# Optimization experiments

Measured on AMD Instinct MI355X. Metric: run time of the kernel, lower is better.

The kernel has to match this reference:

```python
import jax, jax.numpy as jnp
import numpy as np

B, N, C = 4, 2048, 1024
H = 16
HD = C // H
SCALE = HD ** -0.5


def setup_inputs() -> dict:
    key = jax.random.key(0)
    k1, k2, k3, k4 = jax.random.split(key, 4)
    x = jax.random.normal(k1, (B, N, C), dtype=jnp.float32)
    w_qkv = jax.random.normal(k2, (3 * C, C), dtype=jnp.float32) * (C ** -0.5)
    w_proj = jax.random.normal(k3, (C, C), dtype=jnp.float32) * (C ** -0.5)
    b_proj = jax.random.normal(k4, (C,), dtype=jnp.float32) * 0.01
    return {"x": x, "w_qkv": w_qkv, "w_proj": w_proj, "b_proj": b_proj}


def reference(x, w_qkv, w_proj, b_proj):
    qkv = jnp.einsum('bnc,dc->bnd', x, w_qkv)
    qkv = qkv.reshape(B, N, 3, H, HD).transpose(2, 0, 3, 1, 4)
    q, k, v = qkv[0], qkv[1], qkv[2]
    # scaled dot-product attention with explicit softmax (dropout p=0 -> identity)
    attn = jnp.einsum('bhqd,bhkd->bhqk', q, k) * SCALE
    attn = jax.nn.softmax(attn, axis=-1)
    out = jnp.einsum('bhqk,bhkd->bhqd', attn, v)
    out = out.transpose(0, 2, 1, 3).reshape(B, N, C)
    # output projection
    return jnp.einsum('bnc,dc->bnd', out, w_proj) + b_proj
```

## Files before the change

### kernel.cpp

```cpp
#include <hip/hip_runtime.h>

typedef unsigned short u16;
typedef unsigned int u32;
typedef __bf16 bf16x8 __attribute__((ext_vector_type(8)));
typedef __bf16 bf16x4 __attribute__((ext_vector_type(4)));
typedef short s16x4 __attribute__((ext_vector_type(4)));
typedef float f32x4 __attribute__((ext_vector_type(4)));
typedef float f32x16 __attribute__((ext_vector_type(16)));
typedef unsigned int u32x2 __attribute__((ext_vector_type(2)));
typedef unsigned int u32x4 __attribute__((ext_vector_type(4)));

struct __align__(8) u16x4 { u16 x, y, z, w; };

__device__ __forceinline__ void async_copy16(const void* g, void* l) {
  __builtin_amdgcn_global_load_lds(
      (__attribute__((address_space(1))) void*)g,
      (__attribute__((address_space(3))) void*)l, 16, 0, 0);
}

__device__ __forceinline__ u16 f2bf(float f) {
  unsigned u = __builtin_bit_cast(unsigned, f);
  u = (u + 0x7FFFu + ((u >> 16) & 1u)) >> 16;
  return (u16)u;
}
__device__ __forceinline__ float bf2f(u16 h) {
  unsigned u = ((unsigned)h) << 16;
  return __builtin_bit_cast(float, u);
}

__device__ __forceinline__ float fast_exp2(float x) {
  return __builtin_amdgcn_exp2f(x);
}
__device__ __forceinline__ float fast_rcp(float x) {
  return __builtin_amdgcn_rcpf(x);
}

__device__ __forceinline__ f32x4 mfma32(bf16x8 a, bf16x8 b, f32x4 c) {
  return __builtin_amdgcn_mfma_f32_16x16x32_bf16(a, b, c, 0, 0, 0);
}

__device__ __forceinline__ u32 cvt_pk_bf16(float lo, float hi) {
  u32 r;
  asm("v_cvt_pk_bf16_f32 %0, %1, %2" : "=v"(r) : "v"(lo), "v"(hi));
  return r;
}

#define CEXP 0.18033688011112042f

__global__ void detect_mode(const u32* __restrict__ probe, int* __restrict__ flag) {
  __shared__ int cnt[256];
  int t = threadIdx.x;
  int c = 0;
#pragma unroll
  for (int j = 0; j < 16; ++j) {
    u32 v = probe[t + j * 256];
    unsigned e = (v >> 7) & 0xFFu;
    c += (e >= 100u && e <= 130u) ? 1 : 0;
  }
  cnt[t] = c;
  __syncthreads();
  for (int s = 128; s > 0; s >>= 1) {
    if (t < s) cnt[t] += cnt[t + s];
    __syncthreads();
  }
  if (t == 0) *flag = (cnt[0] * 2 > 4096) ? 1 : 0;
}

__global__ void convert_in(const void* __restrict__ src, u16* __restrict__ dst,
                           const int* __restrict__ flag, int n) {
  int mode = *flag;
  int i = (blockIdx.x * blockDim.x + threadIdx.x) * 8;
  if (i >= n) return;
  if (mode == 1) {
    *(uint4*)(dst + i) = *(const uint4*)((const u16*)src + i);
  } else {
    const float* s = (const float*)src;
    float4 a = *(const float4*)(s + i);
    float4 b = *(const float4*)(s + i + 4);
    uint4 o;
    o.x = (u32)f2bf(a.x) | ((u32)f2bf(a.y) << 16);
    o.y = (u32)f2bf(a.z) | ((u32)f2bf(a.w) << 16);
    o.z = (u32)f2bf(b.x) | ((u32)f2bf(b.y) << 16);
    o.w = (u32)f2bf(b.z) | ((u32)f2bf(b.w) << 16);
    *(uint4*)(dst + i) = o;
  }
}

__global__ __launch_bounds__(512, 2) void gemm_bt(
    const u16* __restrict__ A, const u16* __restrict__ Bm,
    u16* __restrict__ C, u16* __restrict__ vT, const u16* __restrict__ bias,
    float* __restrict__ outF, const int* __restrict__ flagp,
    int K, int ldc)
{
  __shared__ __align__(16) char lds[131072];

  const int t = threadIdx.x;
  const int lane = t & 63, wave = t >> 6;
  const int quad = lane >> 4, l16 = lane & 15;
  const int wn = wave & 3, wm = wave >> 2;
  const int rowbase = blockIdx.y * 256;
  const int colbase = blockIdx.x * 256;

  const int srow = t >> 3;
  const int scol = ((t & 7) << 4) ^ ((srow & 7) << 4);
  const int wlds = wave << 10;

  const u16* Arow = A + (size_t)(rowbase + srow) * K + (scol >> 1);
  const u16* Brow = Bm + (size_t)(colbase + srow) * K + (scol >> 1);

  auto stageA = [&](int kb_, int buf_) {
#pragma unroll
    for (int q = 0; q < 4; ++q)
      async_copy16(Arow + (size_t)kb_ * 64 + (size_t)q * 64 * K,
                   lds + buf_ * 32768 + q * 8192 + wlds);
  };
  auto stageB = [&](int kb_, int buf_) {
#pragma unroll
    for (int q = 0; q < 4; ++q)
      async_copy16(Brow + (size_t)kb_ * 64 + (size_t)q * 64 * K,
                   lds + 65536 + buf_ * 32768 + q * 8192 + wlds);
  };

  f32x4 acc[8][4] = {};

  const int swzl = (l16 & 7) << 4;
  const int c0 = (quad * 16) ^ swzl;
  const int c1 = (64 + quad * 16) ^ swzl;
  const char* Ard = lds + (size_t)(wm * 128 + l16) * 128;
  const char* Brd = lds + 65536 + (size_t)(wn * 64 + l16) * 128;

  stageA(0, 0); stageB(0, 0);
  stageA(1, 1); stageB(1, 1);
  asm volatile("s_waitcnt vmcnt(8)" ::: "memory");
  __builtin_amdgcn_s_barrier();

  const int nkb = K >> 6;
  for (int kb = 0; kb < nkb; ++kb) {
    const int cur = kb & 1;
    const char* Ab = Ard + cur * 32768;
    const char* Bb = Brd + cur * 32768;
    bf16x8 aR[4][2], bR[2][2];

#define LOAD_A(ih_)                                                        \
  { _Pragma("unroll") for (int i = 0; i < 4; ++i) {                        \
      aR[i][0] = *(const bf16x8*)(Ab + (ih_) * 8192 + i * 2048 + c0);      \
      aR[i][1] = *(const bf16x8*)(Ab + (ih_) * 8192 + i * 2048 + c1); } }
#define LOAD_B(jh_)                                                        \
  { _Pragma("unroll") for (int j = 0; j < 2; ++j) {                        \
      bR[j][0] = *(const bf16x8*)(Bb + (jh_) * 4096 + j * 2048 + c0);      \
      bR[j][1] = *(const bf16x8*)(Bb + (jh_) * 4096 + j * 2048 + c1); } }
#define MFMA_Q(ih_, jh_)                                                   \
  { __builtin_amdgcn_s_barrier();                                          \
    __builtin_amdgcn_s_setprio(1);                                         \
    _Pragma("unroll") for (int i = 0; i < 4; ++i)                          \
    _Pragma("unroll") for (int j = 0; j < 2; ++j) {                        \
      acc[(ih_) * 4 + i][(jh_) * 2 + j] =                                  \
          mfma32(aR[i][0], bR[j][0], acc[(ih_) * 4 + i][(jh_) * 2 + j]);   \
      acc[(ih_) * 4 + i][(jh_) * 2 + j] =                                  \
          mfma32(aR[i][1], bR[j][1], acc[(ih_) * 4 + i][(jh_) * 2 + j]); } \
    __builtin_amdgcn_s_setprio(0);                                         \
    __builtin_amdgcn_s_barrier(); }

    LOAD_A(0); LOAD_B(0); MFMA_Q(0, 0);
    LOAD_B(1);            MFMA_Q(0, 1);
    LOAD_A(1);            MFMA_Q(1, 1);
    if (kb + 2 < nkb) stageA(kb + 2, cur);
    LOAD_B(0);            MFMA_Q(1, 0);
    if (kb + 2 < nkb) {
      stageB(kb + 2, cur);
      asm volatile("s_waitcnt vmcnt(8)" ::: "memory");
      __builtin_amdgcn_s_barrier();
    } else if (kb + 1 < nkb) {
      asm volatile("s_waitcnt vmcnt(0)" ::: "memory");
      __builtin_amdgcn_s_barrier();
    }
#undef LOAD_A
#undef LOAD_B
#undef MFMA_Q
  }

  if (vT != nullptr && colbase >= 2048) {
#pragma unroll
    for (int mi = 0; mi < 8; ++mi) {
      int rg = rowbase + wm * 128 + mi * 16 + quad * 4;
      int b = rg >> 11, n = rg & 2047;
#pragma unroll
      for (int nj = 0; nj < 4; ++nj) {
        int cg = colbase + wn * 64 + nj * 16 + l16;
        size_t idx = ((size_t)(b * 1024 + (cg - 2048))) * 2048 + n;
        u16x4 pk;
        pk.x = f2bf(acc[mi][nj][0]); pk.y = f2bf(acc[mi][nj][1]);
        pk.z = f2bf(acc[mi][nj][2]); pk.w = f2bf(acc[mi][nj][3]);
        *(u16x4*)(vT + idx) = pk;
      }
    }
  } else {
    const bool f32out = (flagp != nullptr) && (*flagp == 0);
    const float scl = (vT != nullptr && colbase < 1024) ? CEXP : 1.0f;
#pragma unroll
    for (int nj = 0; nj < 4; ++nj) {
      int cg = colbase + wn * 64 + nj * 16 + l16;
      float bv = bias ? bf2f(bias[cg]) : 0.0f;
#pragma unroll
      for (int mi = 0; mi < 8; ++mi) {
#pragma unroll
        for (int r = 0; r < 4; ++r) {
          int rg = rowbase + wm * 128 + mi * 16 + quad * 4 + r;
          float val = acc[mi][nj][r] * scl + bv;
          if (f32out) outF[(size_t)rg * ldc + cg] = val;
          else        C[(size_t)rg * ldc + cg] = f2bf(val);
        }
      }
    }
  }
}

__global__ __launch_bounds__(256, 4) void attn_fwd(
    const u16* __restrict__ qk, const u16* __restrict__ vT, u16* __restrict__ outp)
{
  __shared__ __align__(16) char sm[32768];

  const int t = threadIdx.x;
  const int lane = t & 63, wave = t >> 6;
  const int l31 = lane & 31, h32 = lane >> 5;
  const int bh = blockIdx.x, b = bh >> 4, h = bh & 15;
  const int qtile = blockIdx.y;
  const size_t row0 = (size_t)b * 2048;
  const int qb = qtile * 128 + wave * 32;

  bf16x8 qf[4];
  {
    const u16* qp = qk + (row0 + qb + l31) * 2048 + h * 64 + h32 * 8;
#pragma unroll
    for (int s = 0; s < 4; ++s)
      qf[s] = *(const bf16x8*)(qp + s * 16);
  }

  const u16* Kg[2]; const u16* Vg[2]; unsigned loff[2];
#pragma unroll
  for (int q = 0; q < 2; ++q) {
    int si = q * 256 + t;
    int srow = si >> 3;
    int scolb = ((si & 7) << 4) ^ ((srow & 7) << 4);
    Kg[q] = qk + (row0 + srow) * 2048 + 1024 + h * 64 + (scolb >> 1);
    Vg[q] = vT + ((size_t)(b * 1024 + h * 64 + srow)) * 2048 + (scolb >> 1);
    loff[q] = q * 4096 + wave * 1024;
  }

#pragma unroll
  for (int q = 0; q < 2; ++q) {
    async_copy16(Kg[q], sm + loff[q]);
    async_copy16(Vg[q], sm + 16384 + loff[q]);
  }

  const int swz = (lane & 7) << 4;
  int cswz[4];
#pragma unroll
  for (int s = 0; s < 4; ++s) cswz[s] = (s * 32 + h32 * 16) ^ swz;
  const int rowb = l31 * 128;

  f32x16 o2[2] = {};
  float lsum = 0.0f;

  for (int kb = 0; kb < 32; ++kb) {
    const int cur = kb & 1, nxt = cur ^ 1;
    __syncthreads();
    if (kb < 31) {
#pragma unroll
      for (int q = 0; q < 2; ++q) {
        async_copy16(Kg[q] + (size_t)(kb + 1) * 64 * 2048, sm + nxt * 8192 + loff[q]);
        async_copy16(Vg[q] + (kb + 1) * 64, sm + 16384 + nxt * 8192 + loff[q]);
      }
    }
    const char* Kb = sm + cur * 8192;
    const char* Vb = sm + 16384 + cur * 8192;

#pragma unroll
    for (int kh = 0; kh < 2; ++kh) {
      f32x16 s2 = {};
      __builtin_amdgcn_s_setprio(1);
#pragma unroll
      for (int s = 0; s < 4; ++s) {
        bf16x8 kf = *(const bf16x8*)(Kb + kh * 4096 + rowb + cswz[s]);
        s2 = __builtin_amdgcn_mfma_f32_32x32x16_bf16(kf, qf[s], s2, 0, 0, 0);
      }
      __builtin_amdgcn_s_setprio(0);

      u32 u[8];
#pragma unroll
      for (int w = 0; w < 8; ++w) {
        float p0 = fast_exp2(s2[2 * w]);
        float p1 = fast_exp2(s2[2 * w + 1]);
        lsum += p0 + p1;
        u[w] = cvt_pk_bf16(p0, p1);
      }

      u32x2 r02 = __builtin_amdgcn_permlane32_swap(u[0], u[2], false, false);
      u32x2 r13 = __builtin_amdgcn_permlane32_swap(u[1], u[3], false, false);
      u32x2 r46 = __builtin_amdgcn_permlane32_swap(u[4], u[6], false, false);
      u32x2 r57 = __builtin_amdgcn_permlane32_swap(u[5], u[7], false, false);
      u32x4 fa0v; fa0v.x = r02.x; fa0v.y = r13.x; fa0v.z = r02.y; fa0v.w = r13.y;
      u32x4 fa1v; fa1v.x = r46.x; fa1v.y = r57.x; fa1v.z = r46.y; fa1v.w = r57.y;
      bf16x8 fa0 = __builtin_bit_cast(bf16x8, fa0v);
      bf16x8 fa1 = __builtin_bit_cast(bf16x8, fa1v);

      __builtin_amdgcn_s_setprio(1);
#pragma unroll
      for (int eb = 0; eb < 2; ++eb) {
        bf16x8 v0 = *(const bf16x8*)(Vb + eb * 4096 + rowb + cswz[kh * 2 + 0]);
        o2[eb] = __builtin_amdgcn_mfma_f32_32x32x16_bf16(fa0, v0, o2[eb], 0, 0, 0);
        bf16x8 v1 = *(const bf16x8*)(Vb + eb * 4096 + rowb + cswz[kh * 2 + 1]);
        o2[eb] = __builtin_amdgcn_mfma_f32_32x32x16_bf16(fa1, v1, o2[eb], 0, 0, 0);
      }
      __builtin_amdgcn_s_setprio(0);
    }
  }

  lsum += __shfl_xor(lsum, 32, 64);
  float inv = fast_rcp(lsum);

#pragma unroll
  for (int r = 0; r < 16; ++r) {
    int qr = (r & 3) + 8 * (r >> 2) + 4 * h32;
    float iv = __shfl(inv, qr, 64);
    size_t base = (row0 + qb + qr) * 1024 + h * 64 + l31;
    outp[base]      = f2bf(o2[0][r] * iv);
    outp[base + 32] = f2bf(o2[1][r] * iv);
  }
}

extern "C" void kernel_launch(void* const* d_in, const int* in_sizes, int n_in,
                              void* d_out, int out_size, void* d_ws, size_t ws_size,
                              hipStream_t stream) {
  (void)in_sizes; (void)n_in; (void)out_size; (void)ws_size;
  const void* x_in     = d_in[0];
  const void* wqkv_in  = d_in[1];
  const void* wproj_in = d_in[2];
  const void* bproj_in = d_in[3];

  u16* qkbuf  = (u16*)d_ws;
  u16* vT     = qkbuf + 16777216;
  u16* xb     = vT + 8388608;
  u16* wqkvb  = xb + 8388608;
  int* flag   = (int*)(wqkvb + 3145728);
  u16* attn   = xb;
  u16* wprojb = vT;
  u16* bprojb = vT + 1048576;

  detect_mode<<<1, 256, 0, stream>>>((const u32*)wqkv_in, flag);
  convert_in<<<4096, 256, 0, stream>>>(x_in, xb, flag, 8388608);
  convert_in<<<1536, 256, 0, stream>>>(wqkv_in, wqkvb, flag, 3145728);

  gemm_bt<<<dim3(12, 32), 512, 0, stream>>>(xb, wqkvb, qkbuf, vT, nullptr,
                                            nullptr, nullptr, 1024, 2048);
  attn_fwd<<<dim3(64, 16), 256, 0, stream>>>(qkbuf, vT, attn);

  convert_in<<<512, 256, 0, stream>>>(wproj_in, wprojb, flag, 1048576);
  convert_in<<<1, 256, 0, stream>>>(bproj_in, bprojb, flag, 1024);

  gemm_bt<<<dim3(4, 32), 512, 0, stream>>>(attn, wprojb, (u16*)d_out, nullptr,
                                           bprojb, (float*)d_out, flag, 1024, 1024);
}
```

Baseline: 294.4 us.

## Templatize GEMM N-tile width, add XCD-aware block remap, restructure K-loop

The GEMM kernel is templated on its N-tile width: 192 columns for the QKV projection (512 blocks instead of 384) and 128 for the output projection (256 blocks instead of 128). This gives more workgroups to fill the GPU's compute units, and the smaller tiles shrink LDS use. A block-id remap spreads consecutive tiles across the 8 XCDs. The K-loop now does two half-M MFMA phases, loading all of B once per k-block, and issues the B and A prefetches at different points. The trade is less data reuse per tile and more B and A traffic overall.

```diff
diff --git a/kernel.cpp b/kernel.cpp
--- a/kernel.cpp
+++ b/kernel.cpp
@@ -86,20 +86,25 @@
   }
 }
 
+template<int NJ>
 __global__ __launch_bounds__(512, 2) void gemm_bt(
     const u16* __restrict__ A, const u16* __restrict__ Bm,
     u16* __restrict__ C, u16* __restrict__ vT, const u16* __restrict__ bias,
     float* __restrict__ outF, const int* __restrict__ flagp,
     int K, int ldc)
 {
-  __shared__ __align__(16) char lds[131072];
+  __shared__ __align__(16) char lds[65536 + NJ * 16384];
 
   const int t = threadIdx.x;
   const int lane = t & 63, wave = t >> 6;
   const int quad = lane >> 4, l16 = lane & 15;
   const int wn = wave & 3, wm = wave >> 2;
-  const int rowbase = blockIdx.y * 256;
-  const int colbase = blockIdx.x * 256;
+
+  const int nwg = gridDim.x * gridDim.y;
+  int bid = blockIdx.y * gridDim.x + blockIdx.x;
+  bid = (bid & 7) * (nwg >> 3) + (bid >> 3);
+  const int rowbase = (bid / gridDim.x) * 256;
+  const int colbase = (bid % gridDim.x) * (NJ * 64);
 
   const int srow = t >> 3;
   const int scol = ((t & 7) << 4) ^ ((srow & 7) << 4);
@@ -116,90 +121,100 @@
   };
   auto stageB = [&](int kb_, int buf_) {
 #pragma unroll
-    for (int q = 0; q < 4; ++q)
+    for (int q = 0; q < NJ; ++q)
       async_copy16(Brow + (size_t)kb_ * 64 + (size_t)q * 64 * K,
-                   lds + 65536 + buf_ * 32768 + q * 8192 + wlds);
+                   lds + 65536 + buf_ * (NJ * 8192) + q * 8192 + wlds);
   };
 
-  f32x4 acc[8][4] = {};
+  f32x4 acc[8][NJ] = {};
 
   const int swzl = (l16 & 7) << 4;
   const int c0 = (quad * 16) ^ swzl;
   const int c1 = (64 + quad * 16) ^ swzl;
   const char* Ard = lds + (size_t)(wm * 128 + l16) * 128;
-  const char* Brd = lds + 65536 + (size_t)(wn * 64 + l16) * 128;
+  const char* Brd = lds + 65536 + (size_t)(wn * (NJ * 16) + l16) * 128;
 
   stageA(0, 0); stageB(0, 0);
   stageA(1, 1); stageB(1, 1);
-  asm volatile("s_waitcnt vmcnt(8)" ::: "memory");
+  if constexpr (NJ == 3) asm volatile("s_waitcnt vmcnt(7)" ::: "memory");
+  else                   asm volatile("s_waitcnt vmcnt(6)" ::: "memory");
   __builtin_amdgcn_s_barrier();
 
   const int nkb = K >> 6;
   for (int kb = 0; kb < nkb; ++kb) {
     const int cur = kb & 1;
     const char* Ab = Ard + cur * 32768;
-    const char* Bb = Brd + cur * 32768;
-    bf16x8 aR[4][2], bR[2][2];
-
-#define LOAD_A(ih_)                                                        \
-  { _Pragma("unroll") for (int i = 0; i < 4; ++i) {                        \
-      aR[i][0] = *(const bf16x8*)(Ab + (ih_) * 8192 + i * 2048 + c0);      \
-      aR[i][1] = *(const bf16x8*)(Ab + (ih_) * 8192 + i * 2048 + c1); } }
-#define LOAD_B(jh_)                                                        \
-  { _Pragma("unroll") for (int j = 0; j < 2; ++j) {                        \
-      bR[j][0] = *(const bf16x8*)(Bb + (jh_) * 4096 + j * 2048 + c0);      \
-      bR[j][1] = *(const bf16x8*)(Bb + (jh_) * 4096 + j * 2048 + c1); } }
-#define MFMA_Q(ih_, jh_)                                                   \
-  { __builtin_amdgcn_s_barrier();                                          \
-    __builtin_amdgcn_s_setprio(1);                                         \
-    _Pragma("unroll") for (int i = 0; i < 4; ++i)                          \
-    _Pragma("unroll") for (int j = 0; j < 2; ++j) {                        \
-      acc[(ih_) * 4 + i][(jh_) * 2 + j] =                                  \
-          mfma32(aR[i][0], bR[j][0], acc[(ih_) * 4 + i][(jh_) * 2 + j]);   \
-      acc[(ih_) * 4 + i][(jh_) * 2 + j] =                                  \
-          mfma32(aR[i][1], bR[j][1], acc[(ih_) * 4 + i][(jh_) * 2 + j]); } \
-    __builtin_amdgcn_s_setprio(0);                                         \
-    __builtin_amdgcn_s_barrier(); }
-
-    LOAD_A(0); LOAD_B(0); MFMA_Q(0, 0);
-    LOAD_B(1);            MFMA_Q(0, 1);
-    LOAD_A(1);            MFMA_Q(1, 1);
-    if (kb + 2 < nkb) stageA(kb + 2, cur);
-    LOAD_B(0);            MFMA_Q(1, 0);
+    const char* Bb = Brd + cur * (NJ * 8192);
+    bf16x8 aR[4][2], bR[NJ][2];
+
+#pragma unroll
+    for (int i = 0; i < 4; ++i) {
+      aR[i][0] = *(const bf16x8*)(Ab + i * 2048 + c0);
+      aR[i][1] = *(const bf16x8*)(Ab + i * 2048 + c1);
+    }
+#pragma unroll
+    for (int j = 0; j < NJ; ++j) {
+      bR[j][0] = *(const bf16x8*)(Bb + j * 2048 + c0);
+      bR[j][1] = *(const bf16x8*)(Bb + j * 2048 + c1);
+    }
+    __builtin_amdgcn_s_barrier();
+    __builtin_amdgcn_s_setprio(1);
+#pragma unroll
+    for (int i = 0; i < 4; ++i)
+#pragma unroll
+      for (int j = 0; j < NJ; ++j) {
+        acc[i][j] = mfma32(aR[i][0], bR[j][0], acc[i][j]);
+        acc[i][j] = mfma32(aR[i][1], bR[j][1], acc[i][j]);
+      }
+    __builtin_amdgcn_s_setprio(0);
+    __builtin_amdgcn_s_barrier();
+    if (kb + 2 < nkb) stageB(kb + 2, cur);
+
+#pragma unroll
+    for (int i = 0; i < 4; ++i) {
+      aR[i][0] = *(const bf16x8*)(Ab + 8192 + i * 2048 + c0);
+      aR[i][1] = *(const bf16x8*)(Ab + 8192 + i * 2048 + c1);
+    }
+    __builtin_amdgcn_s_barrier();
+    __builtin_amdgcn_s_setprio(1);
+#pragma unroll
+    for (int i = 0; i < 4; ++i)
+#pragma unroll
+      for (int j = 0; j < NJ; ++j) {
+        acc[4 + i][j] = mfma32(aR[i][0], bR[j][0], acc[4 + i][j]);
+        acc[4 + i][j] = mfma32(aR[i][1], bR[j][1], acc[4 + i][j]);
+      }
+    __builtin_amdgcn_s_setprio(0);
+    __builtin_amdgcn_s_barrier();
+
     if (kb + 2 < nkb) {
-      stageB(kb + 2, cur);
-      asm volatile("s_waitcnt vmcnt(8)" ::: "memory");
+      stageA(kb + 2, cur);
+      if constexpr (NJ == 3) asm volatile("s_waitcnt vmcnt(7)" ::: "memory");
+      else                   asm volatile("s_waitcnt vmcnt(6)" ::: "memory");
       __builtin_amdgcn_s_barrier();
     } else if (kb + 1 < nkb) {
       asm volatile("s_waitcnt vmcnt(0)" ::: "memory");
       __builtin_amdgcn_s_barrier();
     }
-#undef LOAD_A
-#undef LOAD_B
-#undef MFMA_Q
-  }
-
-  if (vT != nullptr && colbase >= 2048) {
-#pragma unroll
-    for (int mi = 0; mi < 8; ++mi) {
-      int rg = rowbase + wm * 128 + mi * 16 + quad * 4;
-      int b = rg >> 11, n = rg & 2047;
-#pragma unroll
-      for (int nj = 0; nj < 4; ++nj) {
-        int cg = colbase + wn * 64 + nj * 16 + l16;
+  }
+
+  const bool f32out = (flagp != nullptr) && (*flagp == 0);
+#pragma unroll
+  for (int nj = 0; nj < NJ; ++nj) {
+    int cg = colbase + wn * (NJ * 16) + nj * 16 + l16;
+    if (vT != nullptr && cg >= 2048) {
+#pragma unroll
+      for (int mi = 0; mi < 8; ++mi) {
+        int rg = rowbase + wm * 128 + mi * 16 + quad * 4;
+        int b = rg >> 11, n = rg & 2047;
         size_t idx = ((size_t)(b * 1024 + (cg - 2048))) * 2048 + n;
         u16x4 pk;
         pk.x = f2bf(acc[mi][nj][0]); pk.y = f2bf(acc[mi][nj][1]);
         pk.z = f2bf(acc[mi][nj][2]); pk.w = f2bf(acc[mi][nj][3]);
         *(u16x4*)(vT + idx) = pk;
       }
-    }
-  } else {
-    const bool f32out = (flagp != nullptr) && (*flagp == 0);
-    const float scl = (vT != nullptr && colbase < 1024) ? CEXP : 1.0f;
-#pragma unroll
-    for (int nj = 0; nj < 4; ++nj) {
-      int cg = colbase + wn * 64 + nj * 16 + l16;
+    } else {
+      const float scl = (vT != nullptr && cg < 1024) ? CEXP : 1.0f;
       float bv = bias ? bf2f(bias[cg]) : 0.0f;
 #pragma unroll
       for (int mi = 0; mi < 8; ++mi) {
@@ -351,13 +366,13 @@
   convert_in<<<4096, 256, 0, stream>>>(x_in, xb, flag, 8388608);
   convert_in<<<1536, 256, 0, stream>>>(wqkv_in, wqkvb, flag, 3145728);
 
-  gemm_bt<<<dim3(12, 32), 512, 0, stream>>>(xb, wqkvb, qkbuf, vT, nullptr,
-                                            nullptr, nullptr, 1024, 2048);
+  gemm_bt<3><<<dim3(16, 32), 512, 0, stream>>>(xb, wqkvb, qkbuf, vT, nullptr,
+                                               nullptr, nullptr, 1024, 2048);
   attn_fwd<<<dim3(64, 16), 256, 0, stream>>>(qkbuf, vT, attn);
 
   convert_in<<<512, 256, 0, stream>>>(wproj_in, wprojb, flag, 1048576);
   convert_in<<<1, 256, 0, stream>>>(bproj_in, bprojb, flag, 1024);
 
-  gemm_bt<<<dim3(4, 32), 512, 0, stream>>>(attn, wprojb, (u16*)d_out, nullptr,
-                                           bprojb, (float*)d_out, flag, 1024, 1024);
-}
+  gemm_bt<2><<<dim3(8, 32), 512, 0, stream>>>(attn, wprojb, (u16*)d_out, nullptr,
+                                              bprojb, (float*)d_out, flag, 1024, 1024);
+}
```

Result: faster. 267.5 us (-9.1%).
